# Optimization experiments

Hardware: AMD Instinct MI355X
Metric: run time of the kernel (lower is better)

## Reference

```python
import jax, jax.numpy as jnp
import numpy as np

TAU = 2.0
THR = 1.0
ALPHA = 10.0
FLOW_SCALE = 16.0  # 2 ** flow_scale_pow2 (=4)
DECAY = 1.0 - 1.0 / TAU


def conv2d(x, w, b=None, stride=1, pad=0):
    # x: [N,C,H,W], w: [O,I,kh,kw]
    out = jax.lax.conv_general_dilated(
        x, w, (stride, stride), [(pad, pad), (pad, pad)],
        dimension_numbers=('NCHW', 'OIHW', 'NCHW'))
    if b is not None:
        out = out + b[None, :, None, None]
    return out


@jax.custom_vjp
def spike(v):
    return (v > 0).astype(v.dtype)

def _spike_fwd(v):
    return (v > 0).astype(v.dtype), v

def _spike_bwd(v, g):
    s = jax.nn.sigmoid(ALPHA * v)
    return (g * ALPHA * s * (1.0 - s),)

spike.defvjp(_spike_fwd, _spike_bwd)


def lif(x, w, b, mem, stride, pad):
    """Conv + leaky-integrate-fire with soft reset. mem init 0 -> first step mem=cur."""
    cur = conv2d(x, w, b, stride, pad)
    mem = mem * DECAY + cur
    s = spike(mem - THR)
    mem = mem - s * THR
    return s, mem


def up2(x):
    return jnp.repeat(jnp.repeat(x, 2, axis=2), 2, axis=3)


def forward(x, w_e1, b_e1, w_e2, b_e2, w_e3, b_e3, w_d3, b_d3,
            w_d2, b_d2, w_d1, b_d1, w_skip2, w_skip1, w_flow, b_flow):
    N, T, C, H, W = x.shape
    bc = w_e1.shape[0]  # base_ch = 32
    z = lambda c, h, w: jnp.zeros((N, c, h, w), x.dtype)
    init = (
        z(bc, H // 2, W // 2),      # mem_e1
        z(2 * bc, H // 4, W // 4),  # mem_e2
        z(4 * bc, H // 8, W // 8),  # mem_e3
        z(2 * bc, H // 4, W // 4),  # mem_d3
        z(bc, H // 2, W // 2),      # mem_d2
        z(bc, H, W),                # mem_d1
        z(bc, H // 2, W // 2),      # mean_e1 (zeros + /(t+1) rule == None-init)
        z(2 * bc, H // 4, W // 4),  # mean_e2
        z(2, H, W),                 # flow_mean
    )

    def step(carry, inp):
        t, xt = inp
        m1, m2, m3, md3, md2, md1, me1, me2, fm = carry
        s1, m1 = lif(xt, w_e1, b_e1, m1, 2, 2)
        s2, m2 = lif(s1, w_e2, b_e2, m2, 2, 1)
        s3, m3 = lif(s2, w_e3, b_e3, m3, 2, 1)
        tf = (t + 1).astype(xt.dtype)
        me1 = me1 + (s1 - me1) / tf
        me2 = me2 + (s2 - me2) / tf
        d3, md3 = lif(up2(s3), w_d3, b_d3, md3, 1, 1)
        d3 = d3 + conv2d(me2, w_skip2)
        d2, md2 = lif(up2(d3), w_d2, b_d2, md2, 1, 1)
        d2 = d2 + conv2d(me1, w_skip1)
        d1, md1 = lif(up2(d2), w_d1, b_d1, md1, 1, 1)
        flow = conv2d(d1, w_flow, b_flow, 1, 1) * FLOW_SCALE
        fm = fm + (flow - fm) / tf
        return (m1, m2, m3, md3, md2, md1, me1, me2, fm), flow

    _, flows = jax.lax.scan(step, init, (jnp.arange(T), jnp.moveaxis(x, 1, 0)))
    return flows[-1]  # return_last_flow=True -> flow of final timestep [N,2,H,W]


def setup_inputs() -> dict:
    key = jax.random.key(0)
    ks = jax.random.split(key, 16)
    N, T, H, W, bc = 4, 8, 256, 256, 32

    def w(k, o, i, kh, kw):
        return jax.random.normal(k, (o, i, kh, kw), jnp.float32) / np.sqrt(i * kh * kw)

    return {
        'x': jax.random.uniform(ks[0], (N, T, 2, H, W), jnp.float32),
        'w_e1': w(ks[1], bc, 2, 5, 5), 'b_e1': jnp.zeros((bc,), jnp.float32),
        'w_e2': w(ks[2], 2 * bc, bc, 3, 3), 'b_e2': jnp.zeros((2 * bc,), jnp.float32),
        'w_e3': w(ks[3], 4 * bc, 2 * bc, 3, 3), 'b_e3': jnp.zeros((4 * bc,), jnp.float32),
        'w_d3': w(ks[4], 2 * bc, 4 * bc, 3, 3), 'b_d3': jnp.zeros((2 * bc,), jnp.float32),
        'w_d2': w(ks[5], bc, 2 * bc, 3, 3), 'b_d2': jnp.zeros((bc,), jnp.float32),
        'w_d1': w(ks[6], bc, bc, 3, 3), 'b_d1': jnp.zeros((bc,), jnp.float32),
        'w_skip2': w(ks[7], 2 * bc, 2 * bc, 1, 1),
        'w_skip1': w(ks[8], bc, bc, 1, 1),
        'w_flow': w(ks[9], 2, bc, 3, 3), 'b_flow': jnp.zeros((2,), jnp.float32),
    }


def reference(x, w_e1, b_e1, w_e2, b_e2, w_e3, b_e3, w_d3, b_d3,
              w_d2, b_d2, w_d1, b_d1, w_skip2, w_skip1, w_flow, b_flow):
    return forward(x, w_e1, b_e1, w_e2, b_e2, w_e3, b_e3, w_d3, b_d3,
                   w_d2, b_d2, w_d1, b_d1, w_skip2, w_skip1, w_flow, b_flow)
```

## Files before the change

### kernel.cpp

```cpp
#include <hip/hip_runtime.h>
#include <cstdint>
#include <cstddef>


static constexpr float THRc   = 1.0f;
static constexpr float DECAYc = 0.5f;

__device__ __forceinline__ float getc(const float4& v, int k) {
    switch (k & 3) {
        case 0: return v.x;
        case 1: return v.y;
        case 2: return v.z;
        default: return v.w;
    }
}

__global__ __launch_bounds__(256) void prep_collapse(const float* __restrict__ w,
                                                     float* __restrict__ wc, int pairs)
{
    int idx = blockIdx.x * 256 + threadIdx.x;
    if (idx >= pairs) return;
    float a[3][3];
#pragma unroll
    for (int i = 0; i < 3; ++i)
#pragma unroll
        for (int j = 0; j < 3; ++j) a[i][j] = w[idx * 9 + i * 3 + j];
    float rs[2][2][3];
#pragma unroll
    for (int kx = 0; kx < 3; ++kx) {
        rs[0][0][kx] = a[0][kx];
        rs[0][1][kx] = a[1][kx] + a[2][kx];
        rs[1][0][kx] = a[0][kx] + a[1][kx];
        rs[1][1][kx] = a[2][kx];
    }
#pragma unroll
    for (int py = 0; py < 2; ++py)
#pragma unroll
        for (int px = 0; px < 2; ++px)
#pragma unroll
            for (int r = 0; r < 2; ++r) {
                float c0, c1;
                if (px == 0) { c0 = rs[py][r][0];               c1 = rs[py][r][1] + rs[py][r][2]; }
                else         { c0 = rs[py][r][0] + rs[py][r][1]; c1 = rs[py][r][2]; }
                wc[idx * 16 + ((py * 2 + px) * 2 + r) * 2 + 0] = c0;
                wc[idx * 16 + ((py * 2 + px) * 2 + r) * 2 + 1] = c1;
            }
}

template<int IC, int ICC, int OC, int SIH, int SIW, int CPT, int YPB, int OCT,
         int NW, int SKIP_IC, int SKC>
__global__ __launch_bounds__(NW * 64) void dec_conv(
    const float* __restrict__ in,
    const float* __restrict__ wc,
    const float* __restrict__ bias,
    float* __restrict__ mem,
    float* __restrict__ out,
    const float* __restrict__ skip_in,
    const float* __restrict__ skip_w)
{
    constexpr int NT   = NW * 64;
    constexpr int LPT  = SIW / CPT;
    static_assert((CPT & 1) == 0 && (CPT == 2 || (CPT & 3) == 0), "CPT even (2 or mult of 4)");
    static_assert(LPT * YPB == 64, "wave must tile the band");
    static_assert((ICC & 1) == 0, "ICC even for wA/wB ping-pong");
    constexpr int OC_B = NW * OCT;
    constexpr int NOCB = OC / OC_B;
    constexpr int NYB  = SIH / YPB;
    constexpr int SP   = SIW + 8;
    constexpr int SR   = YPB + 2;
    constexpr int OH   = 2 * SIH, OW = 2 * SIW;
    constexpr int NCH  = IC / ICC;
    constexpr int W4   = SIW / 4;
    constexpr int TILE = ICC * SR * SP;
    constexpr int OROWS = 2 * YPB;
    constexpr int SKTILE = (SKIP_IC > 0) ? SKC * OROWS * OW : 0;
    constexpr int BASE = (2 * TILE) > SKTILE ? (2 * TILE) : SKTILE;
    constexpr int SLOTS = ICC * SR * W4;

    __shared__ __align__(16) float sb[BASE];

    int b = blockIdx.x;
    const int ocb = b % NOCB; b /= NOCB;
    const int yb  = b % NYB;  b /= NYB;
    const int n   = b;
    const int y0  = yb * YPB;

    const int lane = threadIdx.x & 63;
    const int wav  = threadIdx.x >> 6;
    const int cl   = lane % LPT;
    const int yp   = lane / LPT;
    const int c0   = cl * CPT;
    const int y    = y0 + yp;

    const int oc0 = __builtin_amdgcn_readfirstlane(ocb * OC_B + wav * OCT);

    int lzero;
    asm volatile("v_mov_b32 %0, 0" : "=v"(lzero));
    const float4* wlane = reinterpret_cast<const float4*>(wc) + lzero;
    const int wbase = oc0 * IC * 4;

    for (int f = threadIdx.x; f < 2 * ICC * SR * 2; f += NT) {
        int side = f & 1;
        int t    = f >> 1;
        int r    = t % SR;
        int tt   = t / SR;
        int ic   = tt % ICC;
        int buf  = tt / ICC;
        sb[buf * TILE + (ic * SR + r) * SP + (side ? (SIW + 4) : 3)] = 0.0f;
    }

    float acc[OCT][2][2 * CPT];
#pragma unroll
    for (int j = 0; j < OCT; ++j) {
        float bv = bias[oc0 + j];
#pragma unroll
        for (int py = 0; py < 2; ++py)
#pragma unroll
            for (int q = 0; q < 2 * CPT; ++q) acc[j][py][q] = bv;
    }

    const float* inn = in + (size_t)n * IC * SIH * SIW;

    float4 wA[OCT * 4], wB[OCT * 4];
    auto wload = [&](int icg, float4* dst) {
#pragma unroll
        for (int j = 0; j < OCT; ++j)
#pragma unroll
            for (int g = 0; g < 4; ++g)
                dst[j * 4 + g] = wlane[wbase + (j * IC + icg) * 4 + g];
    };

    auto stage = [&](int buf, int ch) {
        const float* inb = inn + (size_t)ch * ICC * SIH * SIW;
        float* dst = sb + buf * TILE;
        for (int f = threadIdx.x; f < SLOTS; f += NT) {
            int c4 = f & (W4 - 1);
            int t  = f / W4;
            int r  = t % SR;
            int ic = t / SR;
            int sy = y0 - 1 + r;
            float4 v = make_float4(0.f, 0.f, 0.f, 0.f);
            if (sy >= 0 && sy < SIH)
                v = *reinterpret_cast<const float4*>(
                        inb + (size_t)ic * SIH * SIW + (size_t)sy * SIW + 4 * c4);
            *reinterpret_cast<float4*>(&dst[(ic * SR + r) * SP + 4 + 4 * c4]) = v;
        }
    };

    auto compute = [&](const float* bp, int icl, const float4* w) {
        float s[3][CPT + 2];
#pragma unroll
        for (int r = 0; r < 3; ++r) {
            const int rb = (icl * SR + yp + r) * SP;
            s[r][0] = bp[rb + 3 + c0];
            if constexpr (CPT >= 4) {
#pragma unroll
                for (int v = 0; v < CPT / 4; ++v) {
                    float4 t4 = *reinterpret_cast<const float4*>(&bp[rb + 4 + c0 + 4 * v]);
                    s[r][1 + 4 * v] = t4.x; s[r][2 + 4 * v] = t4.y;
                    s[r][3 + 4 * v] = t4.z; s[r][4 + 4 * v] = t4.w;
                }
            } else {
                float2 t2 = *reinterpret_cast<const float2*>(&bp[rb + 4 + c0]);
                s[r][1] = t2.x; s[r][2] = t2.y;
            }
            s[r][CPT + 1] = bp[rb + 4 + c0 + CPT];
        }
#pragma unroll
        for (int j = 0; j < OCT; ++j)
#pragma unroll
            for (int py = 0; py < 2; ++py)
#pragma unroll
                for (int cc = 0; cc < CPT; ++cc)
#pragma unroll
                    for (int px = 0; px < 2; ++px) {
                        float v = acc[j][py][cc * 2 + px];
#pragma unroll
                        for (int rr = 0; rr < 2; ++rr)
#pragma unroll
                            for (int c2 = 0; c2 < 2; ++c2)
                                v += getc(w[j * 4 + py * 2 + px], rr * 2 + c2)
                                   * s[py + rr][cc + px + c2];
                        acc[j][py][cc * 2 + px] = v;
                    }
    };

    wload(0, wA);
    stage(0, 0);
    __syncthreads();
    for (int ch = 0; ch < NCH; ++ch) {
        if (ch + 1 < NCH) stage((ch + 1) & 1, ch + 1);
        const float* bp = sb + (ch & 1) * TILE;
        const int icg0 = ch * ICC;
        for (int ic = 0; ic < ICC; ic += 2) {
            wload(icg0 + ic + 1, wB);
            compute(bp, ic, wA);
            wload(icg0 + ic + 2, wA);
            compute(bp, ic + 1, wB);
        }
        __syncthreads();
    }

    constexpr int NV = (2 * CPT) / 4;
    float sk[OCT][2][2 * CPT] = {};
    if constexpr (SKIP_IC > 0) {
        constexpr int NSK = SKIP_IC / SKC;
        constexpr int OW4 = OW / 4;
        const float* skn = skip_in + (size_t)n * SKIP_IC * OH * OW;
        for (int sc = 0; sc < NSK; ++sc) {
            if (sc) __syncthreads();
            for (int f = threadIdx.x; f < SKC * OROWS * OW4; f += NT) {
                int c4 = f & (OW4 - 1);
                int t  = f / OW4;
                int r  = t % OROWS;
                int ic = t / OROWS;
                *reinterpret_cast<float4*>(&sb[(ic * OROWS + r) * OW + 4 * c4]) =
                    *reinterpret_cast<const float4*>(
                        skn + ((size_t)(sc * SKC + ic) * OH + 2 * y0 + r) * OW + 4 * c4);
            }
            __syncthreads();
            float wsk[OCT][SKC];
#pragma unroll
            for (int j = 0; j < OCT; ++j)
#pragma unroll
                for (int ic = 0; ic < SKC; ++ic)
                    wsk[j][ic] = skip_w[(size_t)(oc0 + j) * SKIP_IC + sc * SKC + ic];
#pragma unroll
            for (int ic = 0; ic < SKC; ++ic)
#pragma unroll
                for (int py = 0; py < 2; ++py)
#pragma unroll
                    for (int v = 0; v < NV; ++v) {
                        float4 sv = *reinterpret_cast<const float4*>(
                            &sb[(ic * OROWS + 2 * yp + py) * OW + 2 * c0 + 4 * v]);
#pragma unroll
                        for (int j = 0; j < OCT; ++j) {
                            sk[j][py][4 * v + 0] += wsk[j][ic] * sv.x;
                            sk[j][py][4 * v + 1] += wsk[j][ic] * sv.y;
                            sk[j][py][4 * v + 2] += wsk[j][ic] * sv.z;
                            sk[j][py][4 * v + 3] += wsk[j][ic] * sv.w;
                        }
                    }
        }
    }

    const bool wout = (out != nullptr);
#pragma unroll
    for (int j = 0; j < OCT; ++j)
#pragma unroll
        for (int py = 0; py < 2; ++py) {
            size_t ob = (((size_t)n * OC + oc0 + j) * OH + (2 * y + py)) * OW + 2 * c0;
#pragma unroll
            for (int v = 0; v < NV; ++v) {
                float4 mv = *reinterpret_cast<const float4*>(&mem[ob + 4 * v]);
                float4 ov, nm;
                float m0 = mv.x * DECAYc + acc[j][py][4 * v + 0];
                float m1 = mv.y * DECAYc + acc[j][py][4 * v + 1];
                float m2 = mv.z * DECAYc + acc[j][py][4 * v + 2];
                float m3 = mv.w * DECAYc + acc[j][py][4 * v + 3];
                float s0 = (m0 - THRc) > 0.0f ? 1.0f : 0.0f;
                float s1 = (m1 - THRc) > 0.0f ? 1.0f : 0.0f;
                float s2 = (m2 - THRc) > 0.0f ? 1.0f : 0.0f;
                float s3 = (m3 - THRc) > 0.0f ? 1.0f : 0.0f;
                nm.x = m0 - s0 * THRc; nm.y = m1 - s1 * THRc;
                nm.z = m2 - s2 * THRc; nm.w = m3 - s3 * THRc;
                *reinterpret_cast<float4*>(&mem[ob + 4 * v]) = nm;
                if (wout) {
                    ov.x = s0 + sk[j][py][4 * v + 0];
                    ov.y = s1 + sk[j][py][4 * v + 1];
                    ov.z = s2 + sk[j][py][4 * v + 2];
                    ov.w = s3 + sk[j][py][4 * v + 3];
                    *reinterpret_cast<float4*>(&out[ob + 4 * v]) = ov;
                }
            }
        }
}

template<int IC, int ICC, int OC, int IH, int IW, int K, int CPT, int LPT, int OCT, bool DO_MEAN>
__global__ __launch_bounds__(256) void enc_conv(
    const float* __restrict__ in, int in_nstride,
    const float* __restrict__ wgt,
    const float* __restrict__ bias,
    float* __restrict__ mem,
    float* __restrict__ out,
    float* __restrict__ mean,
    float inv_tf)
{
    constexpr int P    = K / 2;
    constexpr int OH   = IH / 2, OW = IW / 2;
    constexpr int SPr  = 4 + IW + P;
    constexpr int SP   = (SPr + 3) & ~3;
    constexpr int OC_B = 4 * OCT;
    constexpr int NOCB = OC / OC_B;
    constexpr int RL   = 2 * CPT + 2 * P - 1;
    constexpr int NCH  = IC / ICC;
    constexpr int W4   = IW / 4;
    static_assert(LPT * CPT == OW, "lanes x CPT must cover OW");
    static_assert((ICC & (ICC - 1)) == 0, "ICC pow2");

    __shared__ float sb[K][ICC][SP];

    int b = blockIdx.x;
    const int ocb = b % NOCB; b /= NOCB;
    const int y   = b % OH;   b /= OH;
    const int n   = b;

    const int lane = threadIdx.x & 63;
    const int wav  = threadIdx.x >> 6;
    const int x0   = (lane % LPT) * CPT;
    const int oc0  = __builtin_amdgcn_readfirstlane(ocb * OC_B + wav * OCT);

    for (int f = threadIdx.x; f < K * ICC * 2 * P; f += 256) {
        int h  = f % (2 * P);
        int t  = f / (2 * P);
        int ic = t & (ICC - 1);
        int r  = t / ICC;
        int col = (h < P) ? (4 - P + h) : (4 + IW + h - P);
        sb[r][ic][col] = 0.0f;
    }

    float acc[OCT][CPT];
#pragma unroll
    for (int j = 0; j < OCT; ++j) {
        float bv = bias[oc0 + j];
#pragma unroll
        for (int cc = 0; cc < CPT; ++cc) acc[j][cc] = bv;
    }

    const float* inn = in + (size_t)n * (size_t)in_nstride;

    for (int ch = 0; ch < NCH; ++ch) {
        __syncthreads();
        const float* inb = inn + (size_t)ch * ICC * IH * IW;
        constexpr int SLOTS = K * ICC * W4;
        for (int f = threadIdx.x; f < SLOTS; f += 256) {
            int c4 = f & (W4 - 1);
            int t  = f / W4;
            int ic = t & (ICC - 1);
            int r  = t / ICC;
            int sy = 2 * y - P + r;
            float4 v = make_float4(0.f, 0.f, 0.f, 0.f);
            if (sy >= 0 && sy < IH)
                v = *reinterpret_cast<const float4*>(
                        inb + (size_t)ic * IH * IW + (size_t)sy * IW + 4 * c4);
            *reinterpret_cast<float4*>(&sb[r][ic][4 + 4 * c4]) = v;
        }
        __syncthreads();
        for (int ic = 0; ic < ICC; ++ic) {
            float s[K][RL];
#pragma unroll
            for (int r = 0; r < K; ++r)
#pragma unroll
                for (int k = 0; k < RL; ++k)
                    s[r][k] = sb[r][ic][4 - P + 2 * x0 + k];
            const float* wp = wgt + ((size_t)oc0 * IC + ch * ICC + ic) * (K * K);
#pragma unroll
            for (int j = 0; j < OCT; ++j) {
                float wv[K * K];
#pragma unroll
                for (int k = 0; k < K * K; ++k) wv[k] = wp[(size_t)j * IC * K * K + k];
#pragma unroll
                for (int cc = 0; cc < CPT; ++cc)
#pragma unroll
                    for (int ky = 0; ky < K; ++ky)
#pragma unroll
                        for (int kx = 0; kx < K; ++kx)
                            acc[j][cc] += wv[ky * K + kx] * s[ky][2 * cc + kx];
            }
        }
    }

    if (lane < LPT) {
#pragma unroll
        for (int j = 0; j < OCT; ++j) {
            size_t ob = (((size_t)n * OC + oc0 + j) * OH + y) * OW + x0;
#pragma unroll
            for (int cc = 0; cc < CPT; ++cc) {
                float m  = mem[ob + cc] * DECAYc + acc[j][cc];
                float sp = (m - THRc) > 0.0f ? 1.0f : 0.0f;
                mem[ob + cc] = m - sp * THRc;
                if constexpr (DO_MEAN) {
                    float mv = mean[ob + cc];
                    mean[ob + cc] = mv + (sp - mv) * inv_tf;
                }
                out[ob + cc] = sp;
            }
        }
    }
}

template<int IC, int ICC, int OC, int IH, int IW, int CPT, int LPT, int OCT, bool DO_MEAN>
__global__ __launch_bounds__(256) void enc_convdb(
    const float* __restrict__ in, int in_nstride,
    const float* __restrict__ wgt,
    const float* __restrict__ bias,
    float* __restrict__ mem,
    float* __restrict__ out,
    float* __restrict__ mean,
    float inv_tf)
{
    constexpr int K    = 3;
    constexpr int P    = 1;
    constexpr int OH   = IH / 2, OW = IW / 2;
    constexpr int SPr  = 4 + IW + P;
    constexpr int SP   = (SPr + 3) & ~3;
    constexpr int OC_B = 4 * OCT;
    constexpr int NOCB = OC / OC_B;
    constexpr int RL   = 2 * CPT + 2 * P - 1;
    constexpr int NCH  = IC / ICC;
    constexpr int W4   = IW / 4;
    constexpr int TILE = K * ICC * SP;
    constexpr int SLOTS = K * ICC * W4;
    static_assert(LPT * CPT == OW, "lanes x CPT must cover OW");
    static_assert((ICC & (ICC - 1)) == 0, "ICC pow2");
    static_assert(NCH >= 2, "dbuf needs >=2 chunks");

    __shared__ __align__(16) float sb[2 * TILE];

    int b = blockIdx.x;
    const int ocb = b % NOCB; b /= NOCB;
    const int y   = b % OH;   b /= OH;
    const int n   = b;

    const int lane = threadIdx.x & 63;
    const int wav  = threadIdx.x >> 6;
    const int x0   = (lane % LPT) * CPT;
    const int oc0  = __builtin_amdgcn_readfirstlane(ocb * OC_B + wav * OCT);

    for (int f = threadIdx.x; f < 2 * K * ICC * 2 * P; f += 256) {
        int h   = f % (2 * P);
        int t   = f / (2 * P);
        int ic  = t & (ICC - 1);
        int t2  = t / ICC;
        int r   = t2 % K;
        int buf = t2 / K;
        int col = (h < P) ? (4 - P + h) : (4 + IW + h - P);
        sb[buf * TILE + (r * ICC + ic) * SP + col] = 0.0f;
    }

    float acc[OCT][CPT];
#pragma unroll
    for (int j = 0; j < OCT; ++j) {
        float bv = bias[oc0 + j];
#pragma unroll
        for (int cc = 0; cc < CPT; ++cc) acc[j][cc] = bv;
    }

    const float* inn = in + (size_t)n * (size_t)in_nstride;

    auto stage = [&](int buf, int ch) {
        const float* inb = inn + (size_t)ch * ICC * IH * IW;
        float* dst = sb + buf * TILE;
        for (int f = threadIdx.x; f < SLOTS; f += 256) {
            int c4 = f & (W4 - 1);
            int t  = f / W4;
            int ic = t & (ICC - 1);
            int r  = t / ICC;
            int sy = 2 * y - P + r;
            float4 v = make_float4(0.f, 0.f, 0.f, 0.f);
            if (sy >= 0 && sy < IH)
                v = *reinterpret_cast<const float4*>(
                        inb + (size_t)ic * IH * IW + (size_t)sy * IW + 4 * c4);
            *reinterpret_cast<float4*>(&dst[(r * ICC + ic) * SP + 4 + 4 * c4]) = v;
        }
    };

    stage(0, 0);
    __syncthreads();
    for (int ch = 0; ch < NCH; ++ch) {
        if (ch + 1 < NCH) stage((ch + 1) & 1, ch + 1);
        const float* bp = sb + (ch & 1) * TILE;
        for (int ic = 0; ic < ICC; ++ic) {
            float s[K][RL];
#pragma unroll
            for (int r = 0; r < K; ++r)
#pragma unroll
                for (int k = 0; k < RL; ++k)
                    s[r][k] = bp[(r * ICC + ic) * SP + 4 - P + 2 * x0 + k];
            const float* wp = wgt + ((size_t)oc0 * IC + ch * ICC + ic) * (K * K);
#pragma unroll
            for (int j = 0; j < OCT; ++j) {
                float wv[K * K];
#pragma unroll
                for (int k = 0; k < K * K; ++k) wv[k] = wp[(size_t)j * IC * K * K + k];
#pragma unroll
                for (int cc = 0; cc < CPT; ++cc)
#pragma unroll
                    for (int ky = 0; ky < K; ++ky)
#pragma unroll
                        for (int kx = 0; kx < K; ++kx)
                            acc[j][cc] += wv[ky * K + kx] * s[ky][2 * cc + kx];
            }
        }
        __syncthreads();
    }

    if (lane < LPT) {
#pragma unroll
        for (int j = 0; j < OCT; ++j) {
            size_t ob = (((size_t)n * OC + oc0 + j) * OH + y) * OW + x0;
#pragma unroll
            for (int cc = 0; cc < CPT; ++cc) {
                float m  = mem[ob + cc] * DECAYc + acc[j][cc];
                float sp = (m - THRc) > 0.0f ? 1.0f : 0.0f;
                mem[ob + cc] = m - sp * THRc;
                if constexpr (DO_MEAN) {
                    float mv = mean[ob + cc];
                    mean[ob + cc] = mv + (sp - mv) * inv_tf;
                }
                out[ob + cc] = sp;
            }
        }
    }
}

template<int IC, int OC, int IH, int IW, int OH, int OW,
         int K, int STRIDE, int PAD, bool UP2, int SKIP_IC,
         bool DO_LIF, bool DO_MEAN>
__global__ __launch_bounds__(256) void conv_fused(
    const float* __restrict__ in, int in_nstride,
    const float* __restrict__ wgt,
    const float* __restrict__ bias,
    float* __restrict__ mem,
    float* __restrict__ out,
    const float* __restrict__ skip_in,
    const float* __restrict__ skip_w,
    float* __restrict__ mean,
    float inv_tf, float outscale)
{
    constexpr int VEC  = 4;
    constexpr int OWV  = OW / VEC;
    constexpr int WSZ  = IC * K * K;
    constexpr int SIH  = UP2 ? IH / 2 : IH;
    constexpr int SIW  = UP2 ? IW / 2 : IW;
    constexpr int RLEN = (VEC - 1) * STRIDE + K;

    __shared__ float sw[WSZ];

    const int bstart = blockIdx.x * 256;
    const int oc = (bstart / (OH * OWV)) % OC;

    for (int i = threadIdx.x; i < WSZ; i += 256) sw[i] = wgt[oc * WSZ + i];
    __syncthreads();

    const int idx = bstart + threadIdx.x;
    const int wx  = idx % OWV;
    int tt        = idx / OWV;
    const int oy  = tt % OH; tt /= OH;
    tt /= OC;
    const int n   = tt;
    const int ox0 = wx * VEC;

    const float bv = bias ? bias[oc] : 0.0f;
    float acc[VEC];
#pragma unroll
    for (int v = 0; v < VEC; ++v) acc[v] = bv;

    const float* inn = in + (size_t)n * (size_t)in_nstride;

    for (int ic = 0; ic < IC; ++ic) {
        const float* inc = inn + (size_t)ic * (SIH * SIW);
#pragma unroll
        for (int ky = 0; ky < K; ++ky) {
            const int uy = oy * STRIDE + ky - PAD;
            const bool rowok = (uy >= 0) & (uy < IH);
            int sy = UP2 ? (uy >> 1) : uy;
            sy = sy < 0 ? 0 : (sy > SIH - 1 ? SIH - 1 : sy);
            const float* __restrict__ row = inc + (size_t)sy * SIW;

            float r[RLEN];
#pragma unroll
            for (int j = 0; j < RLEN; ++j) {
                const int ux = ox0 * STRIDE - PAD + j;
                const bool ok = rowok & (ux >= 0) & (ux < IW);
                int sx = UP2 ? (ux >> 1) : ux;
                sx = sx < 0 ? 0 : (sx > SIW - 1 ? SIW - 1 : sx);
                r[j] = ok ? row[sx] : 0.0f;
            }
#pragma unroll
            for (int kx = 0; kx < K; ++kx) {
                const float wv = sw[(ic * K + ky) * K + kx];
#pragma unroll
                for (int v = 0; v < VEC; ++v)
                    acc[v] += r[v * STRIDE + kx] * wv;
            }
        }
    }

    const size_t obase = ((((size_t)n * OC + oc) * OH) + oy) * (size_t)OW + ox0;
#pragma unroll
    for (int v = 0; v < VEC; ++v) out[obase + v] = acc[v] * outscale;
}

extern "C" void kernel_launch(void* const* d_in, const int* in_sizes, int n_in,
                              void* d_out, int out_size, void* d_ws, size_t ws_size,
                              hipStream_t stream)
{
    const float* x     = (const float*)d_in[0];
    const float* w_e1  = (const float*)d_in[1];
    const float* b_e1  = (const float*)d_in[2];
    const float* w_e2  = (const float*)d_in[3];
    const float* b_e2  = (const float*)d_in[4];
    const float* w_e3  = (const float*)d_in[5];
    const float* b_e3  = (const float*)d_in[6];
    const float* w_d3  = (const float*)d_in[7];
    const float* b_d3  = (const float*)d_in[8];
    const float* w_d2  = (const float*)d_in[9];
    const float* b_d2  = (const float*)d_in[10];
    const float* w_d1  = (const float*)d_in[11];
    const float* b_d1  = (const float*)d_in[12];
    const float* w_sk2 = (const float*)d_in[13];
    const float* w_sk1 = (const float*)d_in[14];
    const float* w_fl  = (const float*)d_in[15];
    const float* b_fl  = (const float*)d_in[16];
    float* outp = (float*)d_out;

    float* ws = (float*)d_ws;
    size_t off = 0;
    auto alloc = [&](size_t nelem) { float* p = ws + off; off += nelem; return p; };

    float* m1  = alloc(4UL * 32 * 128 * 128);
    float* m2  = alloc(4UL * 64 * 64 * 64);
    float* m3  = alloc(4UL * 128 * 32 * 32);
    float* md3 = alloc(4UL * 64 * 64 * 64);
    float* md2 = alloc(4UL * 32 * 128 * 128);
    float* md1 = alloc(4UL * 32 * 256 * 256);
    float* me1 = alloc(4UL * 32 * 128 * 128);
    float* me2 = alloc(4UL * 64 * 64 * 64);
    const size_t zcount = off;
    float* s1  = alloc(4UL * 32 * 128 * 128);
    float* s2  = alloc(4UL * 64 * 64 * 64);
    float* s3  = alloc(4UL * 128 * 32 * 32);
    float* d3a = alloc(4UL * 64 * 64 * 64);
    float* d2a = alloc(4UL * 32 * 128 * 128);
    float* d1a = alloc(4UL * 32 * 256 * 256);
    float* wc3 = alloc(64UL * 128 * 16 + 64);
    float* wc2 = alloc(32UL * 64 * 16 + 64);
    float* wc1 = alloc(32UL * 32 * 16 + 64);
    (void)ws_size; (void)in_sizes; (void)n_in; (void)out_size;

    hipMemsetAsync(d_ws, 0, zcount * sizeof(float), stream);

    prep_collapse<<<(64 * 128 + 255) / 256, 256, 0, stream>>>(w_d3, wc3, 64 * 128);
    prep_collapse<<<(32 * 64 + 255) / 256, 256, 0, stream>>>(w_d2, wc2, 32 * 64);
    prep_collapse<<<(32 * 32 + 255) / 256, 256, 0, stream>>>(w_d1, wc1, 32 * 32);

    for (int t = 0; t < 8; ++t) {
        const float inv_tf = 1.0f / (float)(t + 1);
        const float* xt = x + (size_t)t * 2 * 256 * 256;

        enc_conv<2, 2, 32, 256, 256, 5, 2, 64, 2, true>
            <<<4 * 128 * 4, 256, 0, stream>>>(xt, 8 * 2 * 256 * 256, w_e1, b_e1,
                                              m1, s1, me1, inv_tf);
        enc_convdb<32, 8, 64, 128, 128, 1, 64, 2, true>
            <<<4 * 64 * 8, 256, 0, stream>>>(s1, 32 * 128 * 128, w_e2, b_e2,
                                             m2, s2, me2, inv_tf);
        enc_convdb<64, 16, 128, 64, 64, 1, 32, 4, false>
            <<<4 * 32 * 8, 256, 0, stream>>>(s2, 64 * 64 * 64, w_e3, b_e3,
                                             m3, s3, nullptr, inv_tf);
        dec_conv<128, 16, 64, 32, 32, 2, 4, 1, 4, 64, 8>
            <<<4 * 8 * 16, 256, 0, stream>>>(s3, wc3, b_d3, md3, d3a, me2, w_sk2);
        dec_conv<64, 16, 32, 64, 64, 2, 2, 2, 4, 32, 8>
            <<<4 * 32 * 4, 256, 0, stream>>>(d3a, wc2, b_d2, md2, d2a, me1, w_sk1);
        dec_conv<32, 8, 32, 128, 128, 4, 2, 2, 4, 0, 1>
            <<<4 * 64 * 4, 256, 0, stream>>>(d2a, wc1, b_d1, md1,
                                             (t == 7) ? d1a : nullptr, nullptr, nullptr);
        if (t == 7) {
            conv_fused<32, 2, 256, 256, 256, 256, 3, 1, 1, false, 0, false, false>
                <<<512, 256, 0, stream>>>(d1a, 32 * 256 * 256, w_fl, b_fl,
                                          nullptr, outp, nullptr, nullptr, nullptr, inv_tf, 16.0f);
        }
    }
}
```

Baseline: 2.043 ms.

## Software-pipeline timesteps by fusing decoder step t with encoder step t+1

Runs the first timestep's encoder layers before the loop. Each loop iteration then launches three combined kernels that split their blocks between a decoder layer of step t and an encoder layer of step t+1, so the two independent layers share one grid. The running mean me1 is double-buffered so the decoder skip reads step t's mean while the encoder writes step t+1's. The aim is fewer launches and more blocks per launch to fill the GPU. In exchange, each combined kernel takes the larger shared-memory size and register count of its two halves, which may lower occupancy.

After: 2.339 ms. +14.5%, slower.

```diff
diff --git a/kernel.cpp b/kernel.cpp
--- a/kernel.cpp
+++ b/kernel.cpp
@@ -49,7 +49,8 @@
 
 template<int IC, int ICC, int OC, int SIH, int SIW, int CPT, int YPB, int OCT,
          int NW, int SKIP_IC, int SKC>
-__global__ __launch_bounds__(NW * 64) void dec_conv(
+__device__ __forceinline__ void dec_conv_body(
+    int b, float* __restrict__ sb,
     const float* __restrict__ in,
     const float* __restrict__ wc,
     const float* __restrict__ bias,
@@ -60,9 +61,9 @@
 {
     constexpr int NT   = NW * 64;
     constexpr int LPT  = SIW / CPT;
-    static_assert((CPT & 1) == 0 && (CPT == 2 || (CPT & 3) == 0), "CPT even (2 or mult of 4)");
+    static_assert((CPT & 1) == 0 && (CPT == 2 || (CPT & 3) == 0), "CPT even");
     static_assert(LPT * YPB == 64, "wave must tile the band");
-    static_assert((ICC & 1) == 0, "ICC even for wA/wB ping-pong");
+    static_assert((ICC & 1) == 0, "ICC even");
     constexpr int OC_B = NW * OCT;
     constexpr int NOCB = OC / OC_B;
     constexpr int NYB  = SIH / YPB;
@@ -73,13 +74,8 @@
     constexpr int W4   = SIW / 4;
     constexpr int TILE = ICC * SR * SP;
     constexpr int OROWS = 2 * YPB;
-    constexpr int SKTILE = (SKIP_IC > 0) ? SKC * OROWS * OW : 0;
-    constexpr int BASE = (2 * TILE) > SKTILE ? (2 * TILE) : SKTILE;
     constexpr int SLOTS = ICC * SR * W4;
 
-    __shared__ __align__(16) float sb[BASE];
-
-    int b = blockIdx.x;
     const int ocb = b % NOCB; b /= NOCB;
     const int yb  = b % NYB;  b /= NYB;
     const int n   = b;
@@ -277,14 +273,12 @@
 }
 
 template<int IC, int ICC, int OC, int IH, int IW, int K, int CPT, int LPT, int OCT, bool DO_MEAN>
-__global__ __launch_bounds__(256) void enc_conv(
+__device__ __forceinline__ void enc_conv_body(
+    int b, float* __restrict__ sb,
     const float* __restrict__ in, int in_nstride,
-    const float* __restrict__ wgt,
-    const float* __restrict__ bias,
-    float* __restrict__ mem,
-    float* __restrict__ out,
-    float* __restrict__ mean,
-    float inv_tf)
+    const float* __restrict__ wgt, const float* __restrict__ bias,
+    float* __restrict__ mem, float* __restrict__ out,
+    const float* __restrict__ mean_in, float* __restrict__ mean_out, float inv_tf)
 {
     constexpr int P    = K / 2;
     constexpr int OH   = IH / 2, OW = IW / 2;
@@ -298,9 +292,6 @@
     static_assert(LPT * CPT == OW, "lanes x CPT must cover OW");
     static_assert((ICC & (ICC - 1)) == 0, "ICC pow2");
 
-    __shared__ float sb[K][ICC][SP];
-
-    int b = blockIdx.x;
     const int ocb = b % NOCB; b /= NOCB;
     const int y   = b % OH;   b /= OH;
     const int n   = b;
@@ -316,7 +307,7 @@
         int ic = t & (ICC - 1);
         int r  = t / ICC;
         int col = (h < P) ? (4 - P + h) : (4 + IW + h - P);
-        sb[r][ic][col] = 0.0f;
+        sb[(r * ICC + ic) * SP + col] = 0.0f;
     }
 
     float acc[OCT][CPT];
@@ -343,7 +334,7 @@
             if (sy >= 0 && sy < IH)
                 v = *reinterpret_cast<const float4*>(
                         inb + (size_t)ic * IH * IW + (size_t)sy * IW + 4 * c4);
-            *reinterpret_cast<float4*>(&sb[r][ic][4 + 4 * c4]) = v;
+            *reinterpret_cast<float4*>(&sb[(r * ICC + ic) * SP + 4 + 4 * c4]) = v;
         }
         __syncthreads();
         for (int ic = 0; ic < ICC; ++ic) {
@@ -352,7 +343,7 @@
             for (int r = 0; r < K; ++r)
 #pragma unroll
                 for (int k = 0; k < RL; ++k)
-                    s[r][k] = sb[r][ic][4 - P + 2 * x0 + k];
+                    s[r][k] = sb[(r * ICC + ic) * SP + 4 - P + 2 * x0 + k];
             const float* wp = wgt + ((size_t)oc0 * IC + ch * ICC + ic) * (K * K);
 #pragma unroll
             for (int j = 0; j < OCT; ++j) {
@@ -380,8 +371,8 @@
                 float sp = (m - THRc) > 0.0f ? 1.0f : 0.0f;
                 mem[ob + cc] = m - sp * THRc;
                 if constexpr (DO_MEAN) {
-                    float mv = mean[ob + cc];
-                    mean[ob + cc] = mv + (sp - mv) * inv_tf;
+                    float mv = mean_in[ob + cc];
+                    mean_out[ob + cc] = mv + (sp - mv) * inv_tf;
                 }
                 out[ob + cc] = sp;
             }
@@ -390,14 +381,12 @@
 }
 
 template<int IC, int ICC, int OC, int IH, int IW, int CPT, int LPT, int OCT, bool DO_MEAN>
-__global__ __launch_bounds__(256) void enc_convdb(
+__device__ __forceinline__ void enc_convdb_body(
+    int b, float* __restrict__ sb,
     const float* __restrict__ in, int in_nstride,
-    const float* __restrict__ wgt,
-    const float* __restrict__ bias,
-    float* __restrict__ mem,
-    float* __restrict__ out,
-    float* __restrict__ mean,
-    float inv_tf)
+    const float* __restrict__ wgt, const float* __restrict__ bias,
+    float* __restrict__ mem, float* __restrict__ out,
+    const float* __restrict__ mean_in, float* __restrict__ mean_out, float inv_tf)
 {
     constexpr int K    = 3;
     constexpr int P    = 1;
@@ -415,9 +404,6 @@
     static_assert((ICC & (ICC - 1)) == 0, "ICC pow2");
     static_assert(NCH >= 2, "dbuf needs >=2 chunks");
 
-    __shared__ __align__(16) float sb[2 * TILE];
-
-    int b = blockIdx.x;
     const int ocb = b % NOCB; b /= NOCB;
     const int y   = b % OH;   b /= OH;
     const int n   = b;
@@ -505,13 +491,83 @@
                 float sp = (m - THRc) > 0.0f ? 1.0f : 0.0f;
                 mem[ob + cc] = m - sp * THRc;
                 if constexpr (DO_MEAN) {
-                    float mv = mean[ob + cc];
-                    mean[ob + cc] = mv + (sp - mv) * inv_tf;
+                    float mv = mean_in[ob + cc];
+                    mean_out[ob + cc] = mv + (sp - mv) * inv_tf;
                 }
                 out[ob + cc] = sp;
             }
         }
     }
+}
+
+template<int IC, int ICC, int OC, int IH, int IW, int K, int CPT, int LPT, int OCT,
+         bool DO_MEAN, int SMEMW>
+__global__ __launch_bounds__(256) void enc_conv_k(
+    const float* in, int ns, const float* wgt, const float* bias,
+    float* mem, float* out, const float* mean_in, float* mean_out, float inv_tf)
+{
+    __shared__ __align__(16) float smem[SMEMW];
+    enc_conv_body<IC, ICC, OC, IH, IW, K, CPT, LPT, OCT, DO_MEAN>(
+        (int)blockIdx.x, smem, in, ns, wgt, bias, mem, out, mean_in, mean_out, inv_tf);
+}
+
+template<int IC, int ICC, int OC, int IH, int IW, int CPT, int LPT, int OCT,
+         bool DO_MEAN, int SMEMW>
+__global__ __launch_bounds__(256) void enc_convdb_k(
+    const float* in, int ns, const float* wgt, const float* bias,
+    float* mem, float* out, const float* mean_in, float* mean_out, float inv_tf)
+{
+    __shared__ __align__(16) float smem[SMEMW];
+    enc_convdb_body<IC, ICC, OC, IH, IW, CPT, LPT, OCT, DO_MEAN>(
+        (int)blockIdx.x, smem, in, ns, wgt, bias, mem, out, mean_in, mean_out, inv_tf);
+}
+
+__global__ __launch_bounds__(256) void fused_d3_e1(
+    const float* din, const float* dwc, const float* dbias, float* dmem,
+    float* dout, const float* dskip_in, const float* dskip_w,
+    const float* ein, int ens, const float* ew, const float* ebias,
+    float* emem, float* eout, const float* emean_in, float* emean_out, float einv)
+{
+    __shared__ __align__(16) float smem[7680];
+    int b = (int)blockIdx.x;
+    if (b < 512)
+        dec_conv_body<128, 16, 64, 32, 32, 2, 4, 1, 4, 64, 8>(
+            b, smem, din, dwc, dbias, dmem, dout, dskip_in, dskip_w);
+    else
+        enc_conv_body<2, 2, 32, 256, 256, 5, 2, 64, 2, true>(
+            b - 512, smem, ein, ens, ew, ebias, emem, eout, emean_in, emean_out, einv);
+}
+
+__global__ __launch_bounds__(256) void fused_d2_e2(
+    const float* din, const float* dwc, const float* dbias, float* dmem,
+    float* dout, const float* dskip_in, const float* dskip_w,
+    const float* ein, int ens, const float* ew, const float* ebias,
+    float* emem, float* eout, const float* emean_in, float* emean_out, float einv)
+{
+    __shared__ __align__(16) float smem[9216];
+    int b = (int)blockIdx.x;
+    if (b < 512)
+        dec_conv_body<64, 16, 32, 64, 64, 2, 2, 2, 4, 32, 8>(
+            b, smem, din, dwc, dbias, dmem, dout, dskip_in, dskip_w);
+    else
+        enc_convdb_body<32, 8, 64, 128, 128, 1, 64, 2, true>(
+            b - 512, smem, ein, ens, ew, ebias, emem, eout, emean_in, emean_out, einv);
+}
+
+__global__ __launch_bounds__(256) void fused_d1_e3(
+    const float* din, const float* dwc, const float* dbias, float* dmem,
+    float* dout,
+    const float* ein, int ens, const float* ew, const float* ebias,
+    float* emem, float* eout, float einv)
+{
+    __shared__ __align__(16) float smem[8704];
+    int b = (int)blockIdx.x;
+    if (b < 1024)
+        dec_conv_body<32, 8, 32, 128, 128, 4, 2, 2, 4, 0, 1>(
+            b, smem, din, dwc, dbias, dmem, dout, nullptr, nullptr);
+    else
+        enc_convdb_body<64, 16, 128, 64, 64, 1, 32, 4, false>(
+            b - 1024, smem, ein, ens, ew, ebias, emem, eout, nullptr, nullptr, einv);
 }
 
 template<int IC, int OC, int IH, int IW, int OH, int OW,
@@ -619,14 +675,15 @@
     size_t off = 0;
     auto alloc = [&](size_t nelem) { float* p = ws + off; off += nelem; return p; };
 
-    float* m1  = alloc(4UL * 32 * 128 * 128);
-    float* m2  = alloc(4UL * 64 * 64 * 64);
-    float* m3  = alloc(4UL * 128 * 32 * 32);
-    float* md3 = alloc(4UL * 64 * 64 * 64);
-    float* md2 = alloc(4UL * 32 * 128 * 128);
-    float* md1 = alloc(4UL * 32 * 256 * 256);
-    float* me1 = alloc(4UL * 32 * 128 * 128);
-    float* me2 = alloc(4UL * 64 * 64 * 64);
+    float* m1   = alloc(4UL * 32 * 128 * 128);
+    float* m2   = alloc(4UL * 64 * 64 * 64);
+    float* m3   = alloc(4UL * 128 * 32 * 32);
+    float* md3  = alloc(4UL * 64 * 64 * 64);
+    float* md2  = alloc(4UL * 32 * 128 * 128);
+    float* md1  = alloc(4UL * 32 * 256 * 256);
+    float* me1a = alloc(4UL * 32 * 128 * 128);
+    float* me1b = alloc(4UL * 32 * 128 * 128);
+    float* me2  = alloc(4UL * 64 * 64 * 64);
     const size_t zcount = off;
     float* s1  = alloc(4UL * 32 * 128 * 128);
     float* s2  = alloc(4UL * 64 * 64 * 64);
@@ -645,30 +702,40 @@
     prep_collapse<<<(32 * 64 + 255) / 256, 256, 0, stream>>>(w_d2, wc2, 32 * 64);
     prep_collapse<<<(32 * 32 + 255) / 256, 256, 0, stream>>>(w_d1, wc1, 32 * 32);
 
+    float* me1buf[2] = { me1a, me1b };
+
+    enc_conv_k<2, 2, 32, 256, 256, 5, 2, 64, 2, true, 2640>
+        <<<4 * 128 * 4, 256, 0, stream>>>(x, 8 * 2 * 256 * 256, w_e1, b_e1,
+                                          m1, s1, me1buf[0], me1buf[1], 1.0f);
+    enc_convdb_k<32, 8, 64, 128, 128, 1, 64, 2, true, 6528>
+        <<<4 * 64 * 8, 256, 0, stream>>>(s1, 32 * 128 * 128, w_e2, b_e2,
+                                         m2, s2, me2, me2, 1.0f);
+    enc_convdb_k<64, 16, 128, 64, 64, 1, 32, 4, false, 6912>
+        <<<4 * 32 * 8, 256, 0, stream>>>(s2, 64 * 64 * 64, w_e3, b_e3,
+                                         m3, s3, nullptr, nullptr, 1.0f);
+
     for (int t = 0; t < 8; ++t) {
-        const float inv_tf = 1.0f / (float)(t + 1);
-        const float* xt = x + (size_t)t * 2 * 256 * 256;
-
-        enc_conv<2, 2, 32, 256, 256, 5, 2, 64, 2, true>
-            <<<4 * 128 * 4, 256, 0, stream>>>(xt, 8 * 2 * 256 * 256, w_e1, b_e1,
-                                              m1, s1, me1, inv_tf);
-        enc_convdb<32, 8, 64, 128, 128, 1, 64, 2, true>
-            <<<4 * 64 * 8, 256, 0, stream>>>(s1, 32 * 128 * 128, w_e2, b_e2,
-                                             m2, s2, me2, inv_tf);
-        enc_convdb<64, 16, 128, 64, 64, 1, 32, 4, false>
-            <<<4 * 32 * 8, 256, 0, stream>>>(s2, 64 * 64 * 64, w_e3, b_e3,
-                                             m3, s3, nullptr, inv_tf);
-        dec_conv<128, 16, 64, 32, 32, 2, 4, 1, 4, 64, 8>
-            <<<4 * 8 * 16, 256, 0, stream>>>(s3, wc3, b_d3, md3, d3a, me2, w_sk2);
-        dec_conv<64, 16, 32, 64, 64, 2, 2, 2, 4, 32, 8>
-            <<<4 * 32 * 4, 256, 0, stream>>>(d3a, wc2, b_d2, md2, d2a, me1, w_sk1);
-        dec_conv<32, 8, 32, 128, 128, 4, 2, 2, 4, 0, 1>
-            <<<4 * 64 * 4, 256, 0, stream>>>(d2a, wc1, b_d1, md1,
-                                             (t == 7) ? d1a : nullptr, nullptr, nullptr);
-        if (t == 7) {
-            conv_fused<32, 2, 256, 256, 256, 256, 3, 1, 1, false, 0, false, false>
-                <<<512, 256, 0, stream>>>(d1a, 32 * 256 * 256, w_fl, b_fl,
-                                          nullptr, outp, nullptr, nullptr, nullptr, inv_tf, 16.0f);
-        }
-    }
-}
+        const int  t1 = t + 1;
+        const bool he = t1 < 8;
+        const int  xc = he ? t1 : 7;
+        const float einv = 1.0f / (float)(t1 + 1);
+        const float* xt1 = x + (size_t)xc * 2 * 256 * 256;
+        const float* d2skip = me1buf[1 - (t & 1)];
+        const float* e1in  = me1buf[t1 & 1];
+        float*       e1out = me1buf[1 - (t1 & 1)];
+
+        fused_d3_e1<<<he ? 2560 : 512, 256, 0, stream>>>(
+            s3, wc3, b_d3, md3, d3a, me2, w_sk2,
+            xt1, 8 * 2 * 256 * 256, w_e1, b_e1, m1, s1, e1in, e1out, einv);
+        fused_d2_e2<<<he ? 2560 : 512, 256, 0, stream>>>(
+            d3a, wc2, b_d2, md2, d2a, d2skip, w_sk1,
+            s1, 32 * 128 * 128, w_e2, b_e2, m2, s2, me2, me2, einv);
+        fused_d1_e3<<<he ? 2048 : 1024, 256, 0, stream>>>(
+            d2a, wc1, b_d1, md1, (t == 7) ? d1a : nullptr,
+            s2, 64 * 64 * 64, w_e3, b_e3, m3, s3, einv);
+    }
+
+    conv_fused<32, 2, 256, 256, 256, 256, 3, 1, 1, false, 0, false, false>
+        <<<512, 256, 0, stream>>>(d1a, 32 * 256 * 256, w_fl, b_fl,
+                                  nullptr, outp, nullptr, nullptr, nullptr, 1.0f, 16.0f);
+}
```
